# Optimization experiments

Measured on AMD Instinct MI355X. Metric: run time of the kernel, lower is better.

## Reference

```python
import jax, jax.numpy as jnp
import numpy as np

NUM_FREQS = 10
NUM_VOXELS = 512
N_POINTS = 262144
IN_DIM = 3
INPUT_CH = IN_DIM + 2 * NUM_FREQS * IN_DIM  # 63


def posenc(x, num_freqs):
    # NeRF positional encoding: [x, sin(x*2^0), cos(x*2^0), ..., sin(x*2^(F-1)), cos(x*2^(F-1))]
    freqs = (2.0 ** jnp.arange(num_freqs)).astype(x.dtype)           # (F,)
    xf = x[:, None, :] * freqs[None, :, None]                        # (N, F, D)
    sc = jnp.stack([jnp.sin(xf), jnp.cos(xf)], axis=2)               # (N, F, 2, D)
    return jnp.concatenate([x, sc.reshape(x.shape[0], -1)], axis=-1)  # (N, D + 2*F*D)


def setup_inputs() -> dict:
    key = jax.random.key(0)
    k_x, k_w, k_v = jax.random.split(key, 3)
    X = jax.random.normal(k_x, (N_POINTS, IN_DIM), dtype=jnp.float32)
    # linear_mappings reshaped to (3*num_voxels, input_ch), used as Linear weight (no bias)
    W = jax.random.normal(k_w, (3 * NUM_VOXELS, INPUT_CH), dtype=jnp.float32) * 0.02
    row_ids = jnp.arange(N_POINTS, dtype=jnp.int64 if jax.config.jax_enable_x64 else jnp.int32)
    voxel_ids = jax.random.randint(k_v, (N_POINTS,), 0, NUM_VOXELS)
    return {"X": X, "W": W, "row_ids": row_ids, "voxel_ids": voxel_ids}


def reference(X, W, row_ids, voxel_ids):
    encoded_X = posenc(X, NUM_FREQS)                      # (N, 63)
    rgb_clusters = encoded_X @ W.T                        # (N, 3*num_voxels) -- wasteful dense GEMM
    # col_indices per selected row: [3v, 3v+1, 3v+2]
    cols = jnp.stack([3 * voxel_ids, 3 * voxel_ids + 1, 3 * voxel_ids + 2], axis=1)  # (M, 3)
    vals = rgb_clusters[row_ids[:, None], cols]           # (M, 3)
    rgb = jnp.zeros((X.shape[0], 3), dtype=X.dtype)
    rgb = rgb.at[row_ids].set(vals)
    return rgb
```

## Files before the change

kernel.cpp:

```cpp
#include <hip/hip_runtime.h>
#include <math.h>

#define N_POINTS   262144
#define NUM_FREQS  10
#define NUM_VOXELS 512


typedef _Float16 half2v __attribute__((ext_vector_type(2)));

__device__ __forceinline__ half2v u2h(unsigned int u) {
    union { unsigned int u; half2v h; } c; c.u = u; return c.h;
}

__device__ __forceinline__ float dot2acc(half2v a, half2v b, float acc) {
#if __has_builtin(__builtin_amdgcn_fdot2)
    return __builtin_amdgcn_fdot2(a, b, acc, false);
#else
    return acc + (float)a[0] * (float)b[0] + (float)a[1] * (float)b[1];
#endif
}

__global__ __launch_bounds__(1024) void pack_w(
    const float* __restrict__ W, _Float16* __restrict__ Wp)
{
    const int gid = blockIdx.x * 1024 + threadIdx.x;
    const int v = gid / 192, e = gid % 192;
    const int row = e >> 6, col = e & 63;
    Wp[v * 192 + e] = (col < 63) ? (_Float16)W[v * 189 + row * 63 + col]
                                 : (_Float16)0.0f;
}

__device__ __forceinline__ void posenc_pack_dot(
    float x0, float x1, float x2, const _Float16* __restrict__ Wp, int v,
    float& a0, float& a1, float& a2)
{
    half2v eh[32];
#define SETE(p, val) eh[(p) >> 1][(p) & 1] = (_Float16)(val)
    SETE(0, x0); SETE(1, x1); SETE(2, x2);
    SETE(63, 0.0f);

    float s0, c0, s1, c1, s2, c2;
    __sincosf(x0, &s0, &c0);
    __sincosf(x1, &s1, &c1);
    __sincosf(x2, &s2, &c2);
    #pragma unroll
    for (int f = 0; f < NUM_FREQS; ++f) {
        const int b = 3 + 6*f;
        SETE(b+0, s0); SETE(b+1, s1); SETE(b+2, s2);
        SETE(b+3, c0); SETE(b+4, c1); SETE(b+5, c2);
        if (f < NUM_FREQS - 1) {
            const float ns0 = 2.0f*s0*c0, nc0 = c0*c0 - s0*s0;
            const float ns1 = 2.0f*s1*c1, nc1 = c1*c1 - s1*s1;
            const float ns2 = 2.0f*s2*c2, nc2 = c2*c2 - s2*s2;
            s0 = ns0; c0 = nc0; s1 = ns1; c1 = nc1; s2 = ns2; c2 = nc2;
        }
    }
#undef SETE

    const uint4* __restrict__ wb = (const uint4*)(Wp + (size_t)v * 192);
    float acc[3];
    #pragma unroll
    for (int r = 0; r < 3; ++r) {
        float a = 0.0f;
        #pragma unroll
        for (int k = 0; k < 8; ++k) {
            const uint4 q = wb[r * 8 + k];
            a = dot2acc(u2h(q.x), eh[4*k + 0], a);
            a = dot2acc(u2h(q.y), eh[4*k + 1], a);
            a = dot2acc(u2h(q.z), eh[4*k + 2], a);
            a = dot2acc(u2h(q.w), eh[4*k + 3], a);
        }
        acc[r] = a;
    }
    a0 = acc[0]; a1 = acc[1]; a2 = acc[2];
}

__global__ __launch_bounds__(1024) void voxlin_fused(
    const float* __restrict__ X,
    const _Float16* __restrict__ Wp,
    const int* __restrict__ row_ids,
    const int* __restrict__ voxel_ids,
    float* __restrict__ out)
{
    __shared__ float4 pts[1024];
    __shared__ int    hist[NUM_VOXELS];
    __shared__ int    cur[NUM_VOXELS];
    __shared__ int    wsum[8];

    const int t    = threadIdx.x;
    const int lane = t & 63;
    const int wid  = t >> 6;
    const int i    = blockIdx.x * 1024 + t;

    const int   v  = voxel_ids[i];
    const float x0 = X[3*i + 0];
    const float x1 = X[3*i + 1];
    const float x2 = X[3*i + 2];
    const int   r  = row_ids[i];

    if (t < NUM_VOXELS) hist[t] = 0;
    __syncthreads();
    atomicAdd(&hist[v], 1);
    __syncthreads();

    int c = 0, incl = 0;
    if (t < NUM_VOXELS) {
        c = hist[t];
        incl = c;
        #pragma unroll
        for (int d = 1; d < 64; d <<= 1) {
            int n = __shfl_up(incl, d);
            if (lane >= d) incl += n;
        }
        if (lane == 63) wsum[wid] = incl;
    }
    __syncthreads();
    if (t < 64) {
        int s = (lane < 8) ? wsum[lane] : 0;
        #pragma unroll
        for (int d = 1; d < 8; d <<= 1) {
            int n = __shfl_up(s, d);
            if (lane >= d) s += n;
        }
        int excl = __shfl_up(s, 1);
        if (lane == 0) excl = 0;
        if (lane < 8) wsum[lane] = excl;
    }
    __syncthreads();
    if (t < NUM_VOXELS) cur[t] = wsum[wid] + incl - c;
    __syncthreads();

    const int mypos = atomicAdd(&cur[v], 1);
    pts[mypos] = make_float4(x0, x1, x2, __int_as_float(v));
    __syncthreads();

    const float4 q  = pts[t];
    const int    sv = __float_as_int(q.w);
    float a0, a1, a2;
    posenc_pack_dot(q.x, q.y, q.z, Wp, sv, a0, a1, a2);

    pts[t] = make_float4(a0, a1, a2, 0.0f);
    __syncthreads();

    const float4 res = pts[mypos];
    out[3*r + 0] = res.x;
    out[3*r + 1] = res.y;
    out[3*r + 2] = res.z;
}

__global__ __launch_bounds__(256) void voxlin_fallback(
    const float* __restrict__ X, const float* __restrict__ W,
    const int* __restrict__ row_ids, const int* __restrict__ voxel_ids,
    float* __restrict__ out)
{
    const int i = blockIdx.x * 256 + threadIdx.x;
    if (i >= N_POINTS) return;
    const float x0 = X[3*i], x1 = X[3*i+1], x2 = X[3*i+2];
    const int v = voxel_ids[i];
    const float* __restrict__ w0 = W + v * 189;
    const float* __restrict__ w1 = w0 + 63;
    const float* __restrict__ w2 = w0 + 126;
    float a0 = x0*w0[0] + x1*w0[1] + x2*w0[2];
    float a1 = x0*w1[0] + x1*w1[1] + x2*w1[2];
    float a2 = x0*w2[0] + x1*w2[1] + x2*w2[2];
    float s0, c0, s1, c1, s2, c2;
    __sincosf(x0, &s0, &c0); __sincosf(x1, &s1, &c1); __sincosf(x2, &s2, &c2);
    #pragma unroll
    for (int f = 0; f < NUM_FREQS; ++f) {
        const int b = 3 + 6*f;
        a0 += s0*w0[b] + s1*w0[b+1] + s2*w0[b+2] + c0*w0[b+3] + c1*w0[b+4] + c2*w0[b+5];
        a1 += s0*w1[b] + s1*w1[b+1] + s2*w1[b+2] + c0*w1[b+3] + c1*w1[b+4] + c2*w1[b+5];
        a2 += s0*w2[b] + s1*w2[b+1] + s2*w2[b+2] + c0*w2[b+3] + c1*w2[b+4] + c2*w2[b+5];
        if (f < NUM_FREQS - 1) {
            const float ns0 = 2.0f*s0*c0, nc0 = c0*c0 - s0*s0;
            const float ns1 = 2.0f*s1*c1, nc1 = c1*c1 - s1*s1;
            const float ns2 = 2.0f*s2*c2, nc2 = c2*c2 - s2*s2;
            s0 = ns0; c0 = nc0; s1 = ns1; c1 = nc1; s2 = ns2; c2 = nc2;
        }
    }
    const int rr = row_ids[i];
    out[3*rr] = a0; out[3*rr+1] = a1; out[3*rr+2] = a2;
}

extern "C" void kernel_launch(void* const* d_in, const int* in_sizes, int n_in,
                              void* d_out, int out_size, void* d_ws, size_t ws_size,
                              hipStream_t stream) {
    const float* X         = (const float*)d_in[0];
    const float* W         = (const float*)d_in[1];
    const int*   row_ids   = (const int*)d_in[2];
    const int*   voxel_ids = (const int*)d_in[3];
    float*       out       = (float*)d_out;

    const size_t need = (size_t)NUM_VOXELS * 192 * sizeof(_Float16);

    if (ws_size >= need) {
        _Float16* Wp = (_Float16*)d_ws;
        pack_w<<<96, 1024, 0, stream>>>(W, Wp);
        voxlin_fused<<<N_POINTS / 1024, 1024, 0, stream>>>(X, Wp, row_ids, voxel_ids, out);
    } else {
        voxlin_fallback<<<(N_POINTS + 255) / 256, 256, 0, stream>>>(X, W, row_ids, voxel_ids, out);
    }
}
```

Baseline: 70.91 us.

## Halve block size, pack posenc halves with cvt_pkrtz, and reorder padded weight layout

The fused kernel now runs 512-thread blocks with launch bounds (512,4), so the 512-bin voxel scan maps one bin per thread. Each wave also redoes the 8-entry wave-sum scan itself, which drops one barrier. Encoded features are packed two at a time with the packed round-toward-zero f16 convert, and the weight pad slot moves to column 3 so x0..x2 plus the pad fill the first two half2 slots. pack_w writes four halves per thread in one vector store. The trade-offs: each block sorts fewer points, so it gets less voxel locality, and rounding toward zero slightly changes the f16 results.

```diff
diff --git a/kernel.cpp b/kernel.cpp
--- a/kernel.cpp
+++ b/kernel.cpp
@@ -20,14 +20,35 @@
 #endif
 }
 
-__global__ __launch_bounds__(1024) void pack_w(
+__device__ __forceinline__ half2v pkrtz(float a, float b) {
+#if __has_builtin(__builtin_amdgcn_cvt_pkrtz)
+    auto r = __builtin_amdgcn_cvt_pkrtz(a, b);
+    union { decltype(r) r_; half2v h; } c; c.r_ = r; return c.h;
+#else
+    half2v h; h[0] = (_Float16)a; h[1] = (_Float16)b; return h;
+#endif
+}
+
+__global__ __launch_bounds__(256) void pack_w(
     const float* __restrict__ W, _Float16* __restrict__ Wp)
 {
-    const int gid = blockIdx.x * 1024 + threadIdx.x;
-    const int v = gid / 192, e = gid % 192;
-    const int row = e >> 6, col = e & 63;
-    Wp[v * 192 + e] = (col < 63) ? (_Float16)W[v * 189 + row * 63 + col]
-                                 : (_Float16)0.0f;
+    const int gid = blockIdx.x * 256 + threadIdx.x;
+    const int v   = gid / 48;
+    const int e4  = gid % 48;
+    const int row = e4 >> 4;
+    const int g   = e4 & 15;
+    union { _Float16 h[4]; float2 f2; } u;
+    #pragma unroll
+    for (int j = 0; j < 4; ++j) {
+        const int pc = 4 * g + j;
+        float val = 0.0f;
+        if (pc != 3) {
+            const int wc = pc - (pc >= 4);
+            val = W[v * 189 + row * 63 + wc];
+        }
+        u.h[j] = (_Float16)val;
+    }
+    *reinterpret_cast<float2*>(Wp + (size_t)v * 192 + row * 64 + 4 * g) = u.f2;
 }
 
 __device__ __forceinline__ void posenc_pack_dot(
@@ -35,9 +56,8 @@
     float& a0, float& a1, float& a2)
 {
     half2v eh[32];
-#define SETE(p, val) eh[(p) >> 1][(p) & 1] = (_Float16)(val)
-    SETE(0, x0); SETE(1, x1); SETE(2, x2);
-    SETE(63, 0.0f);
+    eh[0] = pkrtz(x0, x1);
+    eh[1] = pkrtz(x2, 0.0f);
 
     float s0, c0, s1, c1, s2, c2;
     __sincosf(x0, &s0, &c0);
@@ -45,9 +65,10 @@
     __sincosf(x2, &s2, &c2);
     #pragma unroll
     for (int f = 0; f < NUM_FREQS; ++f) {
-        const int b = 3 + 6*f;
-        SETE(b+0, s0); SETE(b+1, s1); SETE(b+2, s2);
-        SETE(b+3, c0); SETE(b+4, c1); SETE(b+5, c2);
+        const int b = 2 + 3 * f;
+        eh[b + 0] = pkrtz(s0, s1);
+        eh[b + 1] = pkrtz(s2, c0);
+        eh[b + 2] = pkrtz(c1, c2);
         if (f < NUM_FREQS - 1) {
             const float ns0 = 2.0f*s0*c0, nc0 = c0*c0 - s0*s0;
             const float ns1 = 2.0f*s1*c1, nc1 = c1*c1 - s1*s1;
@@ -55,7 +76,6 @@
             s0 = ns0; c0 = nc0; s1 = ns1; c1 = nc1; s2 = ns2; c2 = nc2;
         }
     }
-#undef SETE
 
     const uint4* __restrict__ wb = (const uint4*)(Wp + (size_t)v * 192);
     float acc[3];
@@ -75,14 +95,14 @@
     a0 = acc[0]; a1 = acc[1]; a2 = acc[2];
 }
 
-__global__ __launch_bounds__(1024) void voxlin_fused(
+__global__ __launch_bounds__(512, 4) void voxlin_fused(
     const float* __restrict__ X,
     const _Float16* __restrict__ Wp,
     const int* __restrict__ row_ids,
     const int* __restrict__ voxel_ids,
     float* __restrict__ out)
 {
-    __shared__ float4 pts[1024];
+    __shared__ float4 pts[512];
     __shared__ int    hist[NUM_VOXELS];
     __shared__ int    cur[NUM_VOXELS];
     __shared__ int    wsum[8];
@@ -90,7 +110,7 @@
     const int t    = threadIdx.x;
     const int lane = t & 63;
     const int wid  = t >> 6;
-    const int i    = blockIdx.x * 1024 + t;
+    const int i    = blockIdx.x * 512 + t;
 
     const int   v  = voxel_ids[i];
     const float x0 = X[3*i + 0];
@@ -98,36 +118,31 @@
     const float x2 = X[3*i + 2];
     const int   r  = row_ids[i];
 
-    if (t < NUM_VOXELS) hist[t] = 0;
+    hist[t] = 0;
     __syncthreads();
     atomicAdd(&hist[v], 1);
     __syncthreads();
 
-    int c = 0, incl = 0;
-    if (t < NUM_VOXELS) {
-        c = hist[t];
-        incl = c;
-        #pragma unroll
-        for (int d = 1; d < 64; d <<= 1) {
-            int n = __shfl_up(incl, d);
-            if (lane >= d) incl += n;
-        }
-        if (lane == 63) wsum[wid] = incl;
-    }
-    __syncthreads();
-    if (t < 64) {
-        int s = (lane < 8) ? wsum[lane] : 0;
-        #pragma unroll
-        for (int d = 1; d < 8; d <<= 1) {
-            int n = __shfl_up(s, d);
-            if (lane >= d) s += n;
-        }
-        int excl = __shfl_up(s, 1);
-        if (lane == 0) excl = 0;
-        if (lane < 8) wsum[lane] = excl;
-    }
-    __syncthreads();
-    if (t < NUM_VOXELS) cur[t] = wsum[wid] + incl - c;
+    const int c = hist[t];
+    int incl = c;
+    #pragma unroll
+    for (int d = 1; d < 64; d <<= 1) {
+        int n = __shfl_up(incl, d);
+        if (lane >= d) incl += n;
+    }
+    if (lane == 63) wsum[wid] = incl;
+    __syncthreads();
+
+    int s8 = (lane < 8) ? wsum[lane] : 0;
+    #pragma unroll
+    for (int d = 1; d < 8; d <<= 1) {
+        int n = __shfl_up(s8, d);
+        if (lane >= d) s8 += n;
+    }
+    int ce = __shfl(s8, (wid == 0) ? 0 : (wid - 1));
+    if (wid == 0) ce = 0;
+
+    cur[t] = ce + incl - c;
     __syncthreads();
 
     const int mypos = atomicAdd(&cur[v], 1);
@@ -195,8 +210,8 @@
 
     if (ws_size >= need) {
         _Float16* Wp = (_Float16*)d_ws;
-        pack_w<<<96, 1024, 0, stream>>>(W, Wp);
-        voxlin_fused<<<N_POINTS / 1024, 1024, 0, stream>>>(X, Wp, row_ids, voxel_ids, out);
+        pack_w<<<96, 256, 0, stream>>>(W, Wp);
+        voxlin_fused<<<512, 512, 0, stream>>>(X, Wp, row_ids, voxel_ids, out);
     } else {
         voxlin_fallback<<<(N_POINTS + 255) / 256, 256, 0, stream>>>(X, W, row_ids, voxel_ids, out);
     }
```

New measurement: 73.06 us. 1.03x slower.
